# Optimization experiments

Hardware: AMD Instinct MI355X
Metric: run time of the kernel (lower is better)

The kernel has to match this reference:

```python
import jax, jax.numpy as jnp
import numpy as np

N_NODES = 50000
N_EDGES = 800000
D_IN = 128
D_HID = 128
D_OUT = 1
N_GRAPHS = 64
NEG_SLOPE = 0.2


def gat_layer(x, src, dst, W, a_src, a_dst, b, n_nodes):
    # x: [N, d_in] -> h: [N, d_hid]
    h = x @ W
    alpha_s = h @ a_src  # [N]
    alpha_d = h @ a_dst  # [N]
    e = jax.nn.leaky_relu(alpha_s[src] + alpha_d[dst], NEG_SLOPE)  # [E]
    # segment softmax over destination neighborhoods
    m = jax.ops.segment_max(e, dst, num_segments=n_nodes)
    ex = jnp.exp(e - m[dst])
    denom = jax.ops.segment_sum(ex, dst, num_segments=n_nodes)
    alpha = ex / (denom[dst] + 1e-16)  # [E]
    out = jax.ops.segment_sum(h[src] * alpha[:, None], dst, num_segments=n_nodes)
    return out + b


def setup_inputs() -> dict:
    key = jax.random.key(0)
    ks = jax.random.split(key, 16)
    x = jax.random.normal(ks[0], (N_NODES, D_IN), dtype=jnp.float32)
    edge_index = jax.random.randint(ks[1], (2, N_EDGES), 0, N_NODES, dtype=jnp.int32)
    batch = jnp.sort(jax.random.randint(ks[2], (N_NODES,), 0, N_GRAPHS, dtype=jnp.int32))
    inp = {"x": x, "edge_index": edge_index, "batch": batch}
    dims = [(D_IN, D_HID), (D_HID, D_HID), (D_HID, D_HID), (D_HID, D_HID)]
    for i, (di, dh) in enumerate(dims, 1):
        kk = jax.random.split(ks[2 + i], 4)
        s = 1.0 / np.sqrt(di)
        inp[f"W{i}"] = jax.random.uniform(kk[0], (di, dh), jnp.float32, -s, s)
        inp[f"a_src{i}"] = jax.random.uniform(kk[1], (dh,), jnp.float32, -s, s)
        inp[f"a_dst{i}"] = jax.random.uniform(kk[2], (dh,), jnp.float32, -s, s)
        inp[f"b{i}"] = jnp.zeros((dh,), jnp.float32)
    s = 1.0 / np.sqrt(D_HID)
    inp["fcW"] = jax.random.uniform(ks[10], (D_HID, D_OUT), jnp.float32, -s, s)
    inp["fcb"] = jnp.zeros((D_OUT,), jnp.float32)
    return inp


def reference(x, edge_index, batch,
              W1, a_src1, a_dst1, b1,
              W2, a_src2, a_dst2, b2,
              W3, a_src3, a_dst3, b3,
              W4, a_src4, a_dst4, b4,
              fcW, fcb):
    n = x.shape[0]
    loops = jnp.arange(n, dtype=edge_index.dtype)
    src = jnp.concatenate([edge_index[0], loops])  # add self-loops (PyG default)
    dst = jnp.concatenate([edge_index[1], loops])
    h = jax.nn.relu(gat_layer(x, src, dst, W1, a_src1, a_dst1, b1, n))
    h = jax.nn.relu(gat_layer(h, src, dst, W2, a_src2, a_dst2, b2, n))
    h = jax.nn.relu(gat_layer(h, src, dst, W3, a_src3, a_dst3, b3, n))
    h = jax.nn.relu(gat_layer(h, src, dst, W4, a_src4, a_dst4, b4, n))
    # global mean pool over graphs
    sums = jax.ops.segment_sum(h, batch, num_segments=N_GRAPHS)
    counts = jax.ops.segment_sum(jnp.ones((n,), h.dtype), batch, num_segments=N_GRAPHS)
    pooled = sums / jnp.maximum(counts, 1.0)[:, None]
    return pooled @ fcW + fcb
```

## Files before the change

kernel.cpp:

```cpp
#include <hip/hip_runtime.h>

#define N_NODES 50000
#define N_EDGES 800000
#define E_TOT (N_EDGES + N_NODES)
#define D 128
#define N_GRAPHS 64
#define NEG_SLOPE 0.2f
#define MAXDEG 256
#define SCAN_BLK 1024
#define SCAN_GRID ((N_NODES + SCAN_BLK - 1) / SCAN_BLK)

typedef _Float16 f16x8 __attribute__((ext_vector_type(8)));
typedef _Float16 f16x2 __attribute__((ext_vector_type(2)));
typedef float f32x4 __attribute__((ext_vector_type(4)));

__device__ __forceinline__ float wave_max(float v) {
  #pragma unroll
  for (int off = 32; off > 0; off >>= 1) v = fmaxf(v, __shfl_xor(v, off));
  return v;
}
__device__ __forceinline__ float wave_sum(float v) {
  #pragma unroll
  for (int off = 32; off > 0; off >>= 1) v += __shfl_xor(v, off);
  return v;
}

__global__ void k_count(const int* __restrict__ ei, int* __restrict__ cnt,
                        unsigned short* __restrict__ rank) {
  int e = blockIdx.x * blockDim.x + threadIdx.x;
  if (e >= E_TOT) return;
  int dst = (e < N_EDGES) ? ei[N_EDGES + e] : (e - N_EDGES);
  rank[e] = (unsigned short)atomicAdd(&cnt[dst], 1);
}

__global__ __launch_bounds__(SCAN_BLK) void k_scan1(const int* __restrict__ cnt,
                                                    int* __restrict__ rowptr,
                                                    int* __restrict__ partial) {
  __shared__ int sm[SCAN_BLK];
  int i = blockIdx.x * SCAN_BLK + threadIdx.x;
  int v = (i < N_NODES) ? cnt[i] : 0;
  sm[threadIdx.x] = v;
  __syncthreads();
  #pragma unroll
  for (int off = 1; off < SCAN_BLK; off <<= 1) {
    int t = (threadIdx.x >= off) ? sm[threadIdx.x - off] : 0;
    __syncthreads();
    sm[threadIdx.x] += t;
    __syncthreads();
  }
  if (i < N_NODES) rowptr[i + 1] = sm[threadIdx.x];
  if (threadIdx.x == SCAN_BLK - 1) partial[blockIdx.x] = sm[threadIdx.x];
}

__global__ void k_scan2(int* __restrict__ partial) {
  int lane = threadIdx.x;
  int v = (lane < SCAN_GRID) ? partial[lane] : 0;
  #pragma unroll
  for (int off = 1; off < 64; off <<= 1) {
    int t = __shfl_up(v, off);
    if (lane >= off) v += t;
  }
  if (lane < SCAN_GRID) partial[lane] = v;
}

__global__ __launch_bounds__(SCAN_BLK) void k_scan3(int* __restrict__ rowptr,
                                                    const int* __restrict__ partial) {
  int i = blockIdx.x * SCAN_BLK + threadIdx.x;
  if (i == 0) rowptr[0] = 0;
  if (i < N_NODES && blockIdx.x > 0) rowptr[i + 1] += partial[blockIdx.x - 1];
}

struct WPtrs {
  const float* w[4];
  _Float16* h[4];
  _Float16* l[4];
};
__global__ __launch_bounds__(256) void k_wconv_all(WPtrs p) {
  int layer = blockIdx.x >> 6;
  int e = (blockIdx.x & 63) * 256 + threadIdx.x;
  int k = e >> 7, n = e & 127;
  float v = p.w[layer][e];
  _Float16 h = (_Float16)v;
  _Float16 lo = (_Float16)(v - (float)h);
  int idx = (n >> 4) * 2048 + (k >> 3) * 128 + (n & 15) * 8 + (k & 7);
  p.h[layer][idx] = h;
  p.l[layer][idx] = lo;
}

template <int MODE>
__global__ __launch_bounds__(256) void k_gemm_mfma(const void* __restrict__ Xv,
                                                   const _Float16* __restrict__ Whf,
                                                   const _Float16* __restrict__ Wlf,
                                                   _Float16* __restrict__ Hh,
                                                   const float* __restrict__ asrc,
                                                   const float* __restrict__ adst,
                                                   float* __restrict__ alpha_s,
                                                   float* __restrict__ alpha_d,
                                                   const int* __restrict__ ei,
                                                   const int* __restrict__ rowptr,
                                                   const unsigned short* __restrict__ rank,
                                                   unsigned short* __restrict__ col) {
  __shared__ __align__(16) _Float16 AhL[8192];
  __shared__ __align__(16) _Float16 AlL[MODE ? 8192 : 1];
  const int tid = threadIdx.x;
  const int l = tid & 63;
  const int w = tid >> 6;
  const int rowbase = blockIdx.x * 64;

  #pragma unroll
  for (int p = 0; p < 4; ++p) {
    int row = p * 16 + (tid >> 4);
    int k0 = (tid & 15) * 8;
    int grow = rowbase + row;
    int idx = (((row >> 4) * 16 + (k0 >> 3)) * 16 + (row & 15)) * 8;
    if (MODE) {
      const float* X = (const float*)Xv;
      float xv[8];
      if (grow < N_NODES) {
        float4 f0 = *reinterpret_cast<const float4*>(&X[(size_t)grow * D + k0]);
        float4 f1 = *reinterpret_cast<const float4*>(&X[(size_t)grow * D + k0 + 4]);
        xv[0] = f0.x; xv[1] = f0.y; xv[2] = f0.z; xv[3] = f0.w;
        xv[4] = f1.x; xv[5] = f1.y; xv[6] = f1.z; xv[7] = f1.w;
      } else {
        #pragma unroll
        for (int j = 0; j < 8; ++j) xv[j] = 0.f;
      }
      f16x8 ah, al;
      #pragma unroll
      for (int j = 0; j < 8; ++j) {
        ah[j] = (_Float16)xv[j];
        al[j] = (_Float16)(xv[j] - (float)ah[j]);
      }
      *reinterpret_cast<f16x8*>(&AhL[idx]) = ah;
      *reinterpret_cast<f16x8*>(&AlL[idx]) = al;
    } else {
      const _Float16* X = (const _Float16*)Xv;
      f16x8 ah = {0, 0, 0, 0, 0, 0, 0, 0};
      if (grow < N_NODES)
        ah = *reinterpret_cast<const f16x8*>(&X[(size_t)grow * D + k0]);
      *reinterpret_cast<f16x8*>(&AhL[idx]) = ah;
    }
  }
  __syncthreads();

  f32x4 acc[8];
  #pragma unroll
  for (int cc = 0; cc < 8; ++cc) acc[cc] = (f32x4){0.f, 0.f, 0.f, 0.f};

  #pragma unroll
  for (int kt = 0; kt < 4; ++kt) {
    int aidx = w * 2048 + kt * 512 + l * 8;
    f16x8 ah = *reinterpret_cast<const f16x8*>(&AhL[aidx]);
    f16x8 al;
    if (MODE) al = *reinterpret_cast<const f16x8*>(&AlL[aidx]);
    #pragma unroll
    for (int cc = 0; cc < 8; ++cc) {
      int bidx = cc * 2048 + kt * 512 + l * 8;
      f16x8 bh = *reinterpret_cast<const f16x8*>(&Whf[bidx]);
      f16x8 bl = *reinterpret_cast<const f16x8*>(&Wlf[bidx]);
      acc[cc] = __builtin_amdgcn_mfma_f32_16x16x32_f16(ah, bh, acc[cc], 0, 0, 0);
      acc[cc] = __builtin_amdgcn_mfma_f32_16x16x32_f16(ah, bl, acc[cc], 0, 0, 0);
      if (MODE)
        acc[cc] = __builtin_amdgcn_mfma_f32_16x16x32_f16(al, bh, acc[cc], 0, 0, 0);
    }
  }

  const int myn = l & 15;
  const int rg4 = l >> 4;
  float asv[8], adv[8];
  #pragma unroll
  for (int cc = 0; cc < 8; ++cc) {
    asv[cc] = asrc[cc * 16 + myn];
    adv[cc] = adst[cc * 16 + myn];
  }
  #pragma unroll
  for (int reg = 0; reg < 4; ++reg) {
    int grow = rowbase + w * 16 + rg4 * 4 + reg;
    float ps = 0.f, pd = 0.f;
    #pragma unroll
    for (int cc = 0; cc < 8; ++cc) {
      float v = acc[cc][reg];
      ps = fmaf(v, asv[cc], ps);
      pd = fmaf(v, adv[cc], pd);
      if (grow < N_NODES) Hh[(size_t)grow * D + cc * 16 + myn] = (_Float16)v;
    }
    #pragma unroll
    for (int off = 1; off < 16; off <<= 1) {
      ps += __shfl_xor(ps, off);
      pd += __shfl_xor(pd, off);
    }
    if (grow < N_NODES && myn == 0) {
      alpha_s[grow] = ps;
      alpha_d[grow] = pd;
    }
  }

  if (MODE) {
    int stride = gridDim.x * blockDim.x;
    for (int e = blockIdx.x * blockDim.x + tid; e < E_TOT; e += stride) {
      int src, dst;
      if (e < N_EDGES) { src = ei[e]; dst = ei[N_EDGES + e]; }
      else { src = e - N_EDGES; dst = src; }
      col[rowptr[dst] + rank[e]] = (unsigned short)src;
    }
  }
}

template <int FINAL>
__global__ __launch_bounds__(256) void k_agg(const _Float16* __restrict__ Hh,
                                             const int* __restrict__ rowptr,
                                             const unsigned short* __restrict__ col,
                                             const float* __restrict__ alpha_s,
                                             const float* __restrict__ alpha_d,
                                             const float* __restrict__ bias,
                                             _Float16* __restrict__ Out,
                                             const float* __restrict__ fcW,
                                             float* __restrict__ ynode) {
  __shared__ float wls[4][MAXDEG];
  __shared__ int cls[4][MAXDEG];
  int wid = threadIdx.x >> 6;
  int lane = threadIdx.x & 63;
  int node = blockIdx.x * 4 + wid;
  if (node >= N_NODES) return;
  int start = rowptr[node], end = rowptr[node + 1];
  int deg = end - start;
  float ad = alpha_d[node];

  float earr[4];
  float m = -1e30f;
  #pragma unroll
  for (int k = 0; k < 4; ++k) {
    int j0 = lane + k * 64;
    earr[k] = -1e30f;
    if (j0 < deg) {
      int s = col[start + j0];
      float e = alpha_s[s] + ad;
      e = e >= 0.f ? e : NEG_SLOPE * e;
      cls[wid][j0] = s;
      earr[k] = e;
    }
  }
  m = fmaxf(fmaxf(earr[0], earr[1]), fmaxf(earr[2], earr[3]));
  for (int j0 = MAXDEG + lane; j0 < deg; j0 += 64) {
    int s = col[start + j0];
    float e = alpha_s[s] + ad;
    e = e >= 0.f ? e : NEG_SLOPE * e;
    m = fmaxf(m, e);
  }
  m = wave_max(m);

  float dsum = 0.f;
  #pragma unroll
  for (int k = 0; k < 4; ++k) {
    int j0 = lane + k * 64;
    if (j0 < deg) {
      float w = expf(earr[k] - m);
      wls[wid][j0] = w;
      dsum += w;
    }
  }
  for (int j0 = MAXDEG + lane; j0 < deg; j0 += 64) {
    int s = col[start + j0];
    float e = alpha_s[s] + ad;
    e = e >= 0.f ? e : NEG_SLOPE * e;
    dsum += expf(e - m);
  }
  dsum = wave_sum(dsum);
  float inv = 1.f / (dsum + 1e-16f);

  float2 acc = make_float2(0.f, 0.f);
  int degc = deg < MAXDEG ? deg : MAXDEG;
  for (int jj = 0; jj < degc; jj += 8) {
    float w[8];
    f16x2 hv[8];
    #pragma unroll
    for (int u = 0; u < 8; ++u) {
      int idx = jj + u;
      bool ok = idx < degc;
      int s = ok ? cls[wid][idx] : cls[wid][0];
      w[u] = ok ? wls[wid][idx] : 0.f;
      hv[u] = *reinterpret_cast<const f16x2*>(&Hh[(size_t)s * D + lane * 2]);
    }
    #pragma unroll
    for (int u = 0; u < 8; ++u) {
      acc.x = fmaf(w[u], (float)hv[u][0], acc.x);
      acc.y = fmaf(w[u], (float)hv[u][1], acc.y);
    }
  }
  for (int jj = MAXDEG; jj < deg; ++jj) {
    int s = col[start + jj];
    float e = alpha_s[s] + ad;
    e = e >= 0.f ? e : NEG_SLOPE * e;
    float w = expf(e - m);
    f16x2 hv = *reinterpret_cast<const f16x2*>(&Hh[(size_t)s * D + lane * 2]);
    acc.x = fmaf(w, (float)hv[0], acc.x);
    acc.y = fmaf(w, (float)hv[1], acc.y);
  }

  float2 bv = *reinterpret_cast<const float2*>(&bias[lane * 2]);
  float ox = fmaxf(acc.x * inv + bv.x, 0.f);
  float oy = fmaxf(acc.y * inv + bv.y, 0.f);
  if (FINAL) {
    float2 wv = *reinterpret_cast<const float2*>(&fcW[lane * 2]);
    float y = wave_sum(ox * wv.x + oy * wv.y);
    if (lane == 0) ynode[node] = y;
  } else {
    f16x2 o;
    o[0] = (_Float16)ox;
    o[1] = (_Float16)oy;
    *reinterpret_cast<f16x2*>(&Out[(size_t)node * D + lane * 2]) = o;
  }
}

__global__ __launch_bounds__(256) void k_final(const float* __restrict__ ynode,
                                               const int* __restrict__ batch,
                                               const float* __restrict__ fcb,
                                               float* __restrict__ out) {
  __shared__ float sm[256];
  int b = blockIdx.x;
  int tid = threadIdx.x;
  int lo = 0, hi = N_NODES;
  while (lo < hi) { int mid = (lo + hi) >> 1; if (batch[mid] < b) lo = mid + 1; else hi = mid; }
  int s0 = lo;
  lo = 0; hi = N_NODES;
  while (lo < hi) { int mid = (lo + hi) >> 1; if (batch[mid] < b + 1) lo = mid + 1; else hi = mid; }
  int s1 = lo;
  float sum = 0.f;
  for (int n = s0 + tid; n < s1; n += 256) sum += ynode[n];
  sm[tid] = sum;
  __syncthreads();
  #pragma unroll
  for (int off = 128; off > 0; off >>= 1) {
    if (tid < off) sm[tid] += sm[tid + off];
    __syncthreads();
  }
  if (tid == 0) out[b] = sm[0] / fmaxf((float)(s1 - s0), 1.f) + fcb[0];
}

extern "C" void kernel_launch(void* const* d_in, const int* in_sizes, int n_in,
                              void* d_out, int out_size, void* d_ws, size_t ws_size,
                              hipStream_t stream) {
  const float* x = (const float*)d_in[0];
  const int* ei = (const int*)d_in[1];
  const int* batch = (const int*)d_in[2];
  const float* W[4]   = {(const float*)d_in[3], (const float*)d_in[7],
                         (const float*)d_in[11], (const float*)d_in[15]};
  const float* asr[4] = {(const float*)d_in[4], (const float*)d_in[8],
                         (const float*)d_in[12], (const float*)d_in[16]};
  const float* adt[4] = {(const float*)d_in[5], (const float*)d_in[9],
                         (const float*)d_in[13], (const float*)d_in[17]};
  const float* bs[4]  = {(const float*)d_in[6], (const float*)d_in[10],
                         (const float*)d_in[14], (const float*)d_in[18]};
  const float* fcW = (const float*)d_in[19];
  const float* fcb = (const float*)d_in[20];
  float* out = (float*)d_out;

  char* ws = (char*)d_ws;
  size_t off = 0;
  _Float16* Hh  = (_Float16*)(ws + off); off += (size_t)N_NODES * D * 2;
  _Float16* hBh = (_Float16*)(ws + off); off += (size_t)N_NODES * D * 2;
  float* alpha_s = (float*)(ws + off); off += (size_t)N_NODES * 4;
  float* alpha_d = (float*)(ws + off); off += (size_t)N_NODES * 4;
  int* cnt  = (int*)(ws + off); off += (size_t)N_NODES * 4;
  int* rowptr = (int*)(ws + off); off += (size_t)(N_NODES + 1) * 4 + 12;
  unsigned short* col = (unsigned short*)(ws + off); off += ((size_t)E_TOT * 2 + 15) & ~15ull;
  unsigned short* rank = (unsigned short*)(ws + off); off += ((size_t)E_TOT * 2 + 15) & ~15ull;
  float* ynode = (float*)(ws + off); off += (size_t)N_NODES * 4;
  int* partial = (int*)(ws + off); off += ((size_t)SCAN_GRID * 4 + 15) & ~15ull;
  _Float16* Whf[4];
  _Float16* Wlf[4];
  for (int lyr = 0; lyr < 4; ++lyr) {
    Whf[lyr] = (_Float16*)(ws + off); off += (size_t)D * D * 2;
    Wlf[lyr] = (_Float16*)(ws + off); off += (size_t)D * D * 2;
  }
  (void)ws_size; (void)in_sizes; (void)n_in; (void)out_size;

  hipMemsetAsync(cnt, 0, (size_t)N_NODES * 4, stream);
  WPtrs wp;
  for (int lyr = 0; lyr < 4; ++lyr) { wp.w[lyr] = W[lyr]; wp.h[lyr] = Whf[lyr]; wp.l[lyr] = Wlf[lyr]; }
  k_wconv_all<<<256, 256, 0, stream>>>(wp);
  int eb = (E_TOT + 255) / 256;
  k_count<<<eb, 256, 0, stream>>>(ei, cnt, rank);
  k_scan1<<<SCAN_GRID, SCAN_BLK, 0, stream>>>(cnt, rowptr, partial);
  k_scan2<<<1, 64, 0, stream>>>(partial);
  k_scan3<<<SCAN_GRID, SCAN_BLK, 0, stream>>>(rowptr, partial);

  int gb = (N_NODES + 63) / 64;
  k_gemm_mfma<1><<<gb, 256, 0, stream>>>(x, Whf[0], Wlf[0], Hh, asr[0], adt[0],
                                         alpha_s, alpha_d, ei, rowptr, rank, col);
  k_agg<0><<<(N_NODES + 3) / 4, 256, 0, stream>>>(Hh, rowptr, col, alpha_s, alpha_d,
                                                  bs[0], hBh, nullptr, nullptr);
  for (int l = 1; l < 4; ++l) {
    k_gemm_mfma<0><<<gb, 256, 0, stream>>>(hBh, Whf[l], Wlf[l], Hh, asr[l], adt[l],
                                           alpha_s, alpha_d, nullptr, nullptr,
                                           nullptr, nullptr);
    if (l < 3) {
      k_agg<0><<<(N_NODES + 3) / 4, 256, 0, stream>>>(Hh, rowptr, col, alpha_s, alpha_d,
                                                      bs[l], hBh, nullptr, nullptr);
    } else {
      k_agg<1><<<(N_NODES + 3) / 4, 256, 0, stream>>>(Hh, rowptr, col, alpha_s, alpha_d,
                                                      bs[l], nullptr, fcW, ynode);
    }
  }
  k_final<<<N_GRAPHS, 256, 0, stream>>>(ynode, batch, fcb, out);
}
```

Before: 297.3 us.

## Split wave into two half-waves gathering two neighbors per step with 8-byte loads

```diff
diff --git a/kernel.cpp b/kernel.cpp
--- a/kernel.cpp
+++ b/kernel.cpp
@@ -11,6 +11,7 @@
 #define SCAN_GRID ((N_NODES + SCAN_BLK - 1) / SCAN_BLK)
 
 typedef _Float16 f16x8 __attribute__((ext_vector_type(8)));
+typedef _Float16 f16x4 __attribute__((ext_vector_type(4)));
 typedef _Float16 f16x2 __attribute__((ext_vector_type(2)));
 typedef float f32x4 __attribute__((ext_vector_type(4)));
 
@@ -217,7 +218,7 @@
                                              const float* __restrict__ fcW,
                                              float* __restrict__ ynode) {
   __shared__ float wls[4][MAXDEG];
-  __shared__ int cls[4][MAXDEG];
+  __shared__ unsigned cls[4][MAXDEG];
   int wid = threadIdx.x >> 6;
   int lane = threadIdx.x & 63;
   int node = blockIdx.x * 4 + wid;
@@ -236,7 +237,7 @@
       int s = col[start + j0];
       float e = alpha_s[s] + ad;
       e = e >= 0.f ? e : NEG_SLOPE * e;
-      cls[wid][j0] = s;
+      cls[wid][j0] = (unsigned)s << 8;
       earr[k] = e;
     }
   }
@@ -268,47 +269,77 @@
   dsum = wave_sum(dsum);
   float inv = 1.f / (dsum + 1e-16f);
 
-  float2 acc = make_float2(0.f, 0.f);
   int degc = deg < MAXDEG ? deg : MAXDEG;
-  for (int jj = 0; jj < degc; jj += 8) {
-    float w[8];
-    f16x2 hv[8];
+  int degc8 = (degc + 7) & ~7;
+  for (int j0 = degc + lane; j0 < degc8; j0 += 64) {
+    cls[wid][j0] = 0;
+    wls[wid][j0] = 0.f;
+  }
+
+  const unsigned fo8 = (unsigned)(lane & 31) * 8;
+  const int e2 = lane >> 5;
+  const char* hbase = (const char*)Hh;
+  f32x4 acc4 = {0.f, 0.f, 0.f, 0.f};
+  for (int jj = 0; jj < degc8; jj += 8) {
+    unsigned offs[4];
+    float w4[4];
+    f16x4 hv[4];
     #pragma unroll
-    for (int u = 0; u < 8; ++u) {
-      int idx = jj + u;
-      bool ok = idx < degc;
-      int s = ok ? cls[wid][idx] : cls[wid][0];
-      w[u] = ok ? wls[wid][idx] : 0.f;
-      hv[u] = *reinterpret_cast<const f16x2*>(&Hh[(size_t)s * D + lane * 2]);
+    for (int u = 0; u < 4; ++u) {
+      int idx = jj + u * 2 + e2;
+      offs[u] = cls[wid][idx] + fo8;
+      w4[u] = wls[wid][idx];
+      hv[u] = *reinterpret_cast<const f16x4*>(hbase + offs[u]);
     }
     #pragma unroll
-    for (int u = 0; u < 8; ++u) {
-      acc.x = fmaf(w[u], (float)hv[u][0], acc.x);
-      acc.y = fmaf(w[u], (float)hv[u][1], acc.y);
-    }
-  }
-  for (int jj = MAXDEG; jj < deg; ++jj) {
-    int s = col[start + jj];
+    for (int u = 0; u < 4; ++u) {
+      acc4.x = fmaf((float)hv[u][0], w4[u], acc4.x);
+      acc4.y = fmaf((float)hv[u][1], w4[u], acc4.y);
+      acc4.z = fmaf((float)hv[u][2], w4[u], acc4.z);
+      acc4.w = fmaf((float)hv[u][3], w4[u], acc4.w);
+    }
+  }
+  for (int jj = MAXDEG; jj < deg; jj += 2) {
+    int idx = jj + e2;
+    bool ok = idx < deg;
+    int s = ok ? (int)col[start + idx] : 0;
     float e = alpha_s[s] + ad;
     e = e >= 0.f ? e : NEG_SLOPE * e;
-    float w = expf(e - m);
-    f16x2 hv = *reinterpret_cast<const f16x2*>(&Hh[(size_t)s * D + lane * 2]);
-    acc.x = fmaf(w, (float)hv[0], acc.x);
-    acc.y = fmaf(w, (float)hv[1], acc.y);
-  }
-
-  float2 bv = *reinterpret_cast<const float2*>(&bias[lane * 2]);
-  float ox = fmaxf(acc.x * inv + bv.x, 0.f);
-  float oy = fmaxf(acc.y * inv + bv.y, 0.f);
+    float w = ok ? expf(e - m) : 0.f;
+    f16x4 hv = *reinterpret_cast<const f16x4*>(hbase + ((unsigned)s << 8) + fo8);
+    acc4.x = fmaf((float)hv[0], w, acc4.x);
+    acc4.y = fmaf((float)hv[1], w, acc4.y);
+    acc4.z = fmaf((float)hv[2], w, acc4.z);
+    acc4.w = fmaf((float)hv[3], w, acc4.w);
+  }
+  acc4.x += __shfl_xor(acc4.x, 32);
+  acc4.y += __shfl_xor(acc4.y, 32);
+  acc4.z += __shfl_xor(acc4.z, 32);
+  acc4.w += __shfl_xor(acc4.w, 32);
+
   if (FINAL) {
-    float2 wv = *reinterpret_cast<const float2*>(&fcW[lane * 2]);
-    float y = wave_sum(ox * wv.x + oy * wv.y);
+    float y = 0.f;
+    if (e2 == 0) {
+      f32x4 bv = *reinterpret_cast<const f32x4*>(&bias[(lane & 31) * 4]);
+      f32x4 wv = *reinterpret_cast<const f32x4*>(&fcW[(lane & 31) * 4]);
+      float o0 = fmaxf(fmaf(acc4.x, inv, bv.x), 0.f);
+      float o1 = fmaxf(fmaf(acc4.y, inv, bv.y), 0.f);
+      float o2 = fmaxf(fmaf(acc4.z, inv, bv.z), 0.f);
+      float o3 = fmaxf(fmaf(acc4.w, inv, bv.w), 0.f);
+      y = o0 * wv.x + o1 * wv.y + o2 * wv.z + o3 * wv.w;
+    }
+    y = wave_sum(y);
     if (lane == 0) ynode[node] = y;
   } else {
-    f16x2 o;
-    o[0] = (_Float16)ox;
-    o[1] = (_Float16)oy;
-    *reinterpret_cast<f16x2*>(&Out[(size_t)node * D + lane * 2]) = o;
+    if (e2 == 0) {
+      f32x4 bv = *reinterpret_cast<const f32x4*>(&bias[(lane & 31) * 4]);
+      f16x4 oh;
+      oh[0] = (_Float16)fmaxf(fmaf(acc4.x, inv, bv.x), 0.f);
+      oh[1] = (_Float16)fmaxf(fmaf(acc4.y, inv, bv.y), 0.f);
+      oh[2] = (_Float16)fmaxf(fmaf(acc4.z, inv, bv.z), 0.f);
+      oh[3] = (_Float16)fmaxf(fmaf(acc4.w, inv, bv.w), 0.f);
+      *reinterpret_cast<f16x4*>((char*)Out + (size_t)node * 256 + fo8) = oh;
+    }
   }
 }
 
```

Result: faster. 291.1 us (-2.1%).
